# Performance work log

Measured on AMD Instinct MI355X. Metric: run time of the kernel, lower is better.

The kernel has to match this reference:

```python
import jax, jax.numpy as jnp
import numpy as np


def setup_inputs() -> dict:
    key = jax.random.key(0)
    k1, k2, k3 = jax.random.split(key, 3)
    x = jax.random.normal(k1, (2, 32, 64, 128, 128), dtype=jnp.float32)  # [B,C,D,H,W]
    # Conv3d(2, 1, 3, padding=1): weight [out=1, in=2, 3,3,3], bias [1]
    fan_in = 2 * 3 * 3 * 3
    bound = 1.0 / np.sqrt(fan_in)
    conv_w = jax.random.uniform(k2, (1, 2, 3, 3, 3), minval=-bound, maxval=bound, dtype=jnp.float32)
    conv_b = jax.random.uniform(k3, (1,), minval=-bound, maxval=bound, dtype=jnp.float32)
    return {"x": x, "conv_w": conv_w, "conv_b": conv_b}


def reference(x, conv_w, conv_b):
    # channel-wise max and mean pooling -> [B,1,D,H,W] each
    max_out = jnp.max(x, axis=1, keepdims=True)
    avg_out = jnp.mean(x, axis=1, keepdims=True)
    pooled = jnp.concatenate([max_out, avg_out], axis=1)  # [B,2,D,H,W]
    # 3x3x3 conv, padding=1, 2->1 channels
    attn = jax.lax.conv_general_dilated(
        pooled, conv_w,
        window_strides=(1, 1, 1),
        padding=((1, 1), (1, 1), (1, 1)),
        dimension_numbers=("NCDHW", "OIDHW", "NCDHW"),
    ) + conv_b[None, :, None, None, None]  # [B,1,D,H,W]
    return x * jax.nn.sigmoid(attn)
```

## Files before the change

kernel.cpp:

```cpp
#include <hip/hip_runtime.h>
#include <math.h>

constexpr int B  = 2;
constexpr int C  = 32;
constexpr int DD = 64;
constexpr int HH = 128;
constexpr int WW = 128;
constexpr int HW   = HH * WW;
constexpr int DHW  = DD * HW;
constexpr int NS   = B * DHW;
constexpr int NS4  = NS / 4;
constexpr int DHW4 = DHW / 4;

typedef float f4 __attribute__((ext_vector_type(4)));

__global__ __launch_bounds__(256) void pool_kernel(
    const float* __restrict__ x,
    float* __restrict__ pmax,
    float* __restrict__ pavg) {
  int idx = blockIdx.x * 256 + threadIdx.x;
  if (idx >= NS4) return;
  int b   = idx / DHW4;
  int sp4 = idx - b * DHW4;

  const f4* xp = (const f4*)x + (size_t)b * C * DHW4 + sp4;
  f4 v  = xp[0];
  f4 mx = v;
  f4 sm = v;
#pragma unroll 8
  for (int c = 1; c < C; ++c) {
    f4 u = xp[(size_t)c * DHW4];
    mx.x = fmaxf(mx.x, u.x); mx.y = fmaxf(mx.y, u.y);
    mx.z = fmaxf(mx.z, u.z); mx.w = fmaxf(mx.w, u.w);
    sm += u;
  }
  ((f4*)pmax)[idx] = mx;
  ((f4*)pavg)[idx] = sm * (1.0f / (float)C);
}

__global__ __launch_bounds__(256) void conv_sig_kernel(
    const float* __restrict__ pmax,
    const float* __restrict__ pavg,
    const float* __restrict__ cw,
    const float* __restrict__ cb,
    float* __restrict__ attn) {
  __shared__ float wsh[54];
  __shared__ float bsh;
  if (threadIdx.x < 54) wsh[threadIdx.x] = cw[threadIdx.x];
  if (threadIdx.x == 0) bsh = cb[0];
  __syncthreads();

  int idx = blockIdx.x * 256 + threadIdx.x;
  if (idx >= NS4) return;
  int b   = idx / DHW4;
  int sp4 = idx - b * DHW4;
  int sp  = sp4 * 4;
  int d   = sp / HW;
  int r   = sp - d * HW;
  int h   = r / WW;
  int w0  = r - h * WW;

  float acc0 = bsh, acc1 = bsh, acc2 = bsh, acc3 = bsh;

#pragma unroll
  for (int ch = 0; ch < 2; ++ch) {
    const float* p  = (ch == 0 ? pmax : pavg) + (size_t)b * DHW;
    const float* wt = wsh + ch * 27;
#pragma unroll
    for (int dd = -1; dd <= 1; ++dd) {
      int zd = d + dd;
      if (zd < 0 || zd >= DD) continue;
#pragma unroll
      for (int hh = -1; hh <= 1; ++hh) {
        int zh = h + hh;
        if (zh < 0 || zh >= HH) continue;
        const float* row = p + zd * HW + zh * WW;
        const float* wr  = wt + (dd + 1) * 9 + (hh + 1) * 3;
        float v[6];
#pragma unroll
        for (int j = 0; j < 6; ++j) {
          int wj = w0 - 1 + j;
          v[j] = (wj >= 0 && wj < WW) ? row[wj] : 0.0f;
        }
#pragma unroll
        for (int t = 0; t < 3; ++t) {
          float wv = wr[t];
          acc0 = fmaf(wv, v[t],     acc0);
          acc1 = fmaf(wv, v[t + 1], acc1);
          acc2 = fmaf(wv, v[t + 2], acc2);
          acc3 = fmaf(wv, v[t + 3], acc3);
        }
      }
    }
  }

  f4 sig;
  sig.x = 1.0f / (1.0f + __expf(-acc0));
  sig.y = 1.0f / (1.0f + __expf(-acc1));
  sig.z = 1.0f / (1.0f + __expf(-acc2));
  sig.w = 1.0f / (1.0f + __expf(-acc3));
  ((f4*)attn)[idx] = sig;
}

__global__ __launch_bounds__(256) void scale_kernel(
    const float* __restrict__ x,
    const float* __restrict__ attn,
    float* __restrict__ out) {
  int idx = blockIdx.x * 256 + threadIdx.x;
  if (idx >= NS4) return;
  int b   = idx / DHW4;
  int sp4 = idx - b * DHW4;

  f4 sig = ((const f4*)attn)[idx];
  const f4* xp = (const f4*)x   + (size_t)b * C * DHW4 + sp4;
  f4*       op = (f4*)out       + (size_t)b * C * DHW4 + sp4;
#pragma unroll 8
  for (int c = 0; c < C; ++c) {
    f4 v = xp[(size_t)c * DHW4];
    v *= sig;
    __builtin_nontemporal_store(v, op + (size_t)c * DHW4);
  }
}

extern "C" void kernel_launch(void* const* d_in, const int* in_sizes, int n_in,
                              void* d_out, int out_size, void* d_ws, size_t ws_size,
                              hipStream_t stream) {
  const float* x  = (const float*)d_in[0];
  const float* cw = (const float*)d_in[1];
  const float* cb = (const float*)d_in[2];
  float* out  = (float*)d_out;
  float* pmax = (float*)d_ws;
  float* pavg = pmax + NS;
  float* attn = pavg + NS;

  dim3 blk(256);
  dim3 grid((NS4 + 255) / 256);
  pool_kernel<<<grid, blk, 0, stream>>>(x, pmax, pavg);
  conv_sig_kernel<<<grid, blk, 0, stream>>>(pmax, pavg, cw, cb, attn);
  scale_kernel<<<grid, blk, 0, stream>>>(x, attn, out);
}
```

Before: 553.4 us.

## Fuse pooling, conv-sigmoid and scaling into a cooperative kernel with grid sync

Replaces the three-kernel pipeline with a single cooperative kernel. It computes the channel max/mean, does a grid-wide sync, then runs the 3x3x3 conv, the sigmoid and the channel scaling without writing an attention buffer. If the cooperative launch fails, it falls back to two kernels with conv, sigmoid and scale fused. This removes the attention map round trip and one or two launches. In exchange, launch_bounds(256,8) limits registers, there is a grid-sync cost, and all 2048 blocks must be co-resident for the cooperative launch to succeed.

```diff
diff --git a/kernel.cpp b/kernel.cpp
--- a/kernel.cpp
+++ b/kernel.cpp
@@ -1,5 +1,8 @@
 #include <hip/hip_runtime.h>
+#include <hip/hip_cooperative_groups.h>
 #include <math.h>
+
+namespace cg = cooperative_groups;
 
 constexpr int B  = 2;
 constexpr int C  = 32;
@@ -14,6 +17,97 @@
 
 typedef float f4 __attribute__((ext_vector_type(4)));
 
+__global__ __launch_bounds__(256, 8) void fused_kernel(
+    const float* __restrict__ x,
+    const float* __restrict__ cw,
+    const float* __restrict__ cb,
+    float* __restrict__ pmax,
+    float* __restrict__ pavg,
+    float* __restrict__ out) {
+  __shared__ float wsh[54];
+  __shared__ float bsh;
+  if (threadIdx.x < 54) wsh[threadIdx.x] = cw[threadIdx.x];
+  if (threadIdx.x == 0) bsh = cb[0];
+
+  const int idx = blockIdx.x * 256 + threadIdx.x;
+  const int b   = idx / DHW4;
+  const int sp4 = idx - b * DHW4;
+
+  {
+    const f4* xp = (const f4*)x + (size_t)b * C * DHW4 + sp4;
+    f4 v  = xp[0];
+    f4 mx = v;
+    f4 sm = v;
+#pragma unroll 8
+    for (int c = 1; c < C; ++c) {
+      f4 u = xp[(size_t)c * DHW4];
+      mx.x = fmaxf(mx.x, u.x); mx.y = fmaxf(mx.y, u.y);
+      mx.z = fmaxf(mx.z, u.z); mx.w = fmaxf(mx.w, u.w);
+      sm += u;
+    }
+    ((f4*)pmax)[idx] = mx;
+    ((f4*)pavg)[idx] = sm * (1.0f / (float)C);
+  }
+
+  __threadfence();
+  cg::this_grid().sync();
+
+  const int sp = sp4 * 4;
+  const int d  = sp / HW;
+  const int r  = sp - d * HW;
+  const int h  = r / WW;
+  const int w0 = r - h * WW;
+
+  float acc0 = bsh, acc1 = bsh, acc2 = bsh, acc3 = bsh;
+
+#pragma unroll
+  for (int ch = 0; ch < 2; ++ch) {
+    const float* p  = (ch == 0 ? pmax : pavg) + (size_t)b * DHW;
+    const float* wt = wsh + ch * 27;
+#pragma unroll
+    for (int dd = -1; dd <= 1; ++dd) {
+      int zd = d + dd;
+      if (zd < 0 || zd >= DD) continue;
+#pragma unroll
+      for (int hh = -1; hh <= 1; ++hh) {
+        int zh = h + hh;
+        if (zh < 0 || zh >= HH) continue;
+        const float* row = p + zd * HW + zh * WW;
+        const float* wr  = wt + (dd + 1) * 9 + (hh + 1) * 3;
+        float v[6];
+#pragma unroll
+        for (int j = 0; j < 6; ++j) {
+          int wj = w0 - 1 + j;
+          v[j] = (wj >= 0 && wj < WW) ? row[wj] : 0.0f;
+        }
+#pragma unroll
+        for (int t = 0; t < 3; ++t) {
+          float wv = wr[t];
+          acc0 = fmaf(wv, v[t],     acc0);
+          acc1 = fmaf(wv, v[t + 1], acc1);
+          acc2 = fmaf(wv, v[t + 2], acc2);
+          acc3 = fmaf(wv, v[t + 3], acc3);
+        }
+      }
+    }
+  }
+
+  f4 sig;
+  sig.x = 1.0f / (1.0f + __expf(-acc0));
+  sig.y = 1.0f / (1.0f + __expf(-acc1));
+  sig.z = 1.0f / (1.0f + __expf(-acc2));
+  sig.w = 1.0f / (1.0f + __expf(-acc3));
+
+  const f4* xp = (const f4*)x   + (size_t)b * C * DHW4 + sp4;
+  f4*       op = (f4*)out       + (size_t)b * C * DHW4 + sp4;
+#pragma unroll 8
+  for (int c = 0; c < C; ++c) {
+    f4 v = xp[(size_t)c * DHW4];
+    v *= sig;
+    __builtin_nontemporal_store(v, op + (size_t)c * DHW4);
+  }
+}
+
 __global__ __launch_bounds__(256) void pool_kernel(
     const float* __restrict__ x,
     float* __restrict__ pmax,
@@ -38,12 +132,13 @@
   ((f4*)pavg)[idx] = sm * (1.0f / (float)C);
 }
 
-__global__ __launch_bounds__(256) void conv_sig_kernel(
+__global__ __launch_bounds__(256) void attn_scale_kernel(
+    const float* __restrict__ x,
     const float* __restrict__ pmax,
     const float* __restrict__ pavg,
     const float* __restrict__ cw,
     const float* __restrict__ cb,
-    float* __restrict__ attn) {
+    float* __restrict__ out) {
   __shared__ float wsh[54];
   __shared__ float bsh;
   if (threadIdx.x < 54) wsh[threadIdx.x] = cw[threadIdx.x];
@@ -99,19 +194,7 @@
   sig.y = 1.0f / (1.0f + __expf(-acc1));
   sig.z = 1.0f / (1.0f + __expf(-acc2));
   sig.w = 1.0f / (1.0f + __expf(-acc3));
-  ((f4*)attn)[idx] = sig;
-}
-
-__global__ __launch_bounds__(256) void scale_kernel(
-    const float* __restrict__ x,
-    const float* __restrict__ attn,
-    float* __restrict__ out) {
-  int idx = blockIdx.x * 256 + threadIdx.x;
-  if (idx >= NS4) return;
-  int b   = idx / DHW4;
-  int sp4 = idx - b * DHW4;
-
-  f4 sig = ((const f4*)attn)[idx];
+
   const f4* xp = (const f4*)x   + (size_t)b * C * DHW4 + sp4;
   f4*       op = (f4*)out       + (size_t)b * C * DHW4 + sp4;
 #pragma unroll 8
@@ -131,11 +214,16 @@
   float* out  = (float*)d_out;
   float* pmax = (float*)d_ws;
   float* pavg = pmax + NS;
-  float* attn = pavg + NS;
 
   dim3 blk(256);
-  dim3 grid((NS4 + 255) / 256);
-  pool_kernel<<<grid, blk, 0, stream>>>(x, pmax, pavg);
-  conv_sig_kernel<<<grid, blk, 0, stream>>>(pmax, pavg, cw, cb, attn);
-  scale_kernel<<<grid, blk, 0, stream>>>(x, attn, out);
-}
+  dim3 grid(NS4 / 256);
+
+  void* args[] = {(void*)&x, (void*)&cw, (void*)&cb,
+                  (void*)&pmax, (void*)&pavg, (void*)&out};
+  hipError_t err = hipLaunchCooperativeKernel((const void*)fused_kernel,
+                                              grid, blk, args, 0, stream);
+  if (err != hipSuccess) {
+    pool_kernel<<<grid, blk, 0, stream>>>(x, pmax, pavg);
+    attn_scale_kernel<<<grid, blk, 0, stream>>>(x, pmax, pavg, cw, cb, out);
+  }
+}
```

Measured after the change: 1.093 ms. 1.98x slower.
